# Optimization experiments

Measured on AMD Instinct MI355X. Metric: run time of the kernel, lower is better.

## Reference

```python
import jax, jax.numpy as jnp
import numpy as np

B, T, Q, H = 128, 50, 1024, 256
MAX_STEP = 50
TEMP = 0.5
SUP_W, DIST_W, EMBED_W, LOSS_WEIGHT = 1.0, 0.01, 1.0, 1.0
BLUR, DIAMETER, REACH, SCALING, P = 0.005, 1.0, 500.0, 0.5, 2
NEG = -1e9


def _softmin(eps, C, h):
    # h: log-weights + potential/eps over the second axis of C
    return -eps * jax.nn.logsumexp(h[None, :] - C / eps, axis=1)


def _sqcost(u, v):
    sq = jnp.sum(u * u, -1)[:, None] + jnp.sum(v * v, -1)[None, :] - 2.0 * (u @ v.T)
    return 0.5 * jnp.maximum(sq, 0.0)  # geomloss p=2 cost: |x-y|^2 / 2


def sinkhorn_divergence(x, y):
    # geomloss SamplesLoss('sinkhorn', p=2, blur=0.005, diameter=1, reach=500),
    # tensorized, debiased, unbalanced, eps-scaling schedule.
    N, M = x.shape[0], y.shape[0]
    a_log = jnp.full((N,), -np.log(float(N)), dtype=x.dtype)
    b_log = jnp.full((M,), -np.log(float(M)), dtype=x.dtype)
    Cxy, Cyx = _sqcost(x, y), _sqcost(y, x)
    Cxx, Cyy = _sqcost(x, x), _sqcost(y, y)
    rho = REACH ** P
    eps_final = BLUR ** P
    eps_list = []
    e = DIAMETER ** P
    while e > eps_final:
        eps_list.append(e)
        e = e * (SCALING ** P)
    eps_list.append(eps_final)
    f_ab = jnp.zeros((N,), x.dtype)
    g_ab = jnp.zeros((M,), x.dtype)
    f_aa = jnp.zeros((N,), x.dtype)
    g_bb = jnp.zeros((M,), x.dtype)
    for eps in eps_list:  # static schedule (~9 steps)
        damp = 1.0 / (1.0 + eps / rho)
        ft = damp * _softmin(eps, Cxy, b_log + g_ab / eps)
        gt = damp * _softmin(eps, Cyx, a_log + f_ab / eps)
        faa = 0.5 * (f_aa + damp * _softmin(eps, Cxx, a_log + f_aa / eps))
        gbb = 0.5 * (g_bb + damp * _softmin(eps, Cyy, b_log + g_bb / eps))
        f_ab, g_ab, f_aa, g_bb = ft, gt, faa, gbb
    w = rho + eps_final / 2.0  # UnbalancedWeight
    a_w, b_w = jnp.exp(a_log), jnp.exp(b_log)
    return (jnp.sum(a_w * w * (jnp.exp(-f_aa / rho) - jnp.exp(-f_ab / rho)))
            + jnp.sum(b_w * w * (jnp.exp(-g_bb / rho) - jnp.exp(-g_ab / rho))))


def _forward(lc, lt, le, ltc, ltt, lte, ohs, oht, ods, odt, batch):
    p_c, p_t, p_e = lc / TEMP, lt / TEMP, le / TEMP
    q_c, q_t, q_e = ltc / TEMP, ltt / TEMP, lte / TEMP
    flat = lambda z: z.reshape(z.shape[0], -1)
    loss_kd = (sinkhorn_divergence(flat(p_c), flat(q_c))
               + sinkhorn_divergence(flat(p_t), flat(q_t))
               + sinkhorn_divergence(flat(p_e), flat(q_e)))
    S = MAX_STEP - 1
    delta = batch[:, :, :Q] + batch[:, :, Q:]  # [B,T,Q] question one-hots
    a = jnp.floor(((batch[:, :, :Q] - batch[:, :, Q:]).sum(-1) + 1.0) / 2.0)[:, 1:1 + S]  # [B,S] correctness
    dsh = delta[:, 1:1 + S]  # [B,S,Q]
    # diagonal of p[:S] @ delta[1:].T == per-step gather of next question's logit
    pc = jnp.einsum('bsq,bsq->bs', p_c[:, :S], dsh)
    pt = jnp.einsum('bsq,bsq->bs', p_t[:, :S], dsh)
    pe = jnp.einsum('bsq,bsq->bs', p_e[:, :S], dsh)
    idx = jnp.arange(S)
    last = jnp.max(jnp.where(pc > 0, idx[None, :], -1), axis=1)  # last i with pc[i] > 0
    L = jnp.where(last >= 0, last + 1, S)  # no break => keep full length
    mask = idx[None, :] < L[:, None]
    def ce(logits):
        m = jnp.where(mask, logits, NEG)
        lsm = m - jax.nn.logsumexp(m, axis=1, keepdims=True)
        return -jnp.sum(jnp.where(mask, a * lsm, 0.0))  # soft-target CE, summed over students
    loss_sup = ce(pt) + ce(pc) + ce(pe)
    embed = 0.5 * (jnp.sum((ohs - oht) ** 2) + jnp.sum((ods - odt) ** 2))
    total = LOSS_WEIGHT * (SUP_W * loss_sup + DIST_W * loss_kd + EMBED_W * embed)
    return total.reshape(1)


def setup_inputs():
    key = jax.random.key(0)
    ks = jax.random.split(key, 12)
    rn = lambda k, s: jax.random.normal(k, s, dtype=jnp.float32)
    qid = jax.random.randint(ks[10], (B, T), 0, Q)
    correct = jax.random.randint(ks[11], (B, T), 0, 2).astype(jnp.float32)
    oh = jax.nn.one_hot(qid, Q, dtype=jnp.float32)
    batch = jnp.concatenate([oh * correct[..., None], oh * (1.0 - correct)[..., None]], axis=-1)
    return {
        'logit_c': rn(ks[0], (B, T, Q)),
        'logit_t': rn(ks[1], (B, T, Q)),
        'logit_ensemble': rn(ks[2], (B, T, Q)),
        'logit_teacher_c': rn(ks[3], (B, T, Q)),
        'logit_teacher_t': rn(ks[4], (B, T, Q)),
        'logit_teacher_ensemble': rn(ks[5], (B, T, Q)),
        'out_h_student': rn(ks[6], (B, T, H)),
        'out_h_teacher': rn(ks[7], (B, T, H)),
        'out_d_student': rn(ks[8], (B, T, H)),
        'out_d_teacher': rn(ks[9], (B, T, H)),
        'batch': batch,
    }


def reference(logit_c, logit_t, logit_ensemble, logit_teacher_c, logit_teacher_t, logit_teacher_ensemble, out_h_student, out_h_teacher, out_d_student, out_d_teacher, batch):
    return _forward(logit_c, logit_t, logit_ensemble, logit_teacher_c, logit_teacher_t, logit_teacher_ensemble, out_h_student, out_h_teacher, out_d_student, out_d_teacher, batch)
```

## Files before the change

kernel.cpp:

```cpp
#include <hip/hip_runtime.h>

#define NB 128
#define T_DIM 50
#define Q_DIM 1024
#define H_DIM 256
#define S_DIM 49
#define K_DIM 51200
#define KCHUNKS 80
#define KC 640
#define BK 64
#define NSTAGE 10
#define GRAM_N (NB * NB)
#define LROWU 36
#define CPAD 132

typedef __attribute__((ext_vector_type(4))) float f32x4;
typedef __attribute__((ext_vector_type(8))) _Float16 half8v;
typedef __attribute__((ext_vector_type(4))) unsigned int uint4v;
typedef __attribute__((ext_vector_type(2))) unsigned int uint2v;
using pk2_t = decltype(__builtin_amdgcn_cvt_pkrtz(0.0f, 0.0f));

union PKU { pk2_t p; unsigned int u; };
union U4H8 { uint4v u; half8v h; };

__device__ inline unsigned short f2bf_rn(float x) {
  union { float f; unsigned int u; } v; v.f = x;
  unsigned int r = v.u + 0x7FFFu + ((v.u >> 16) & 1u);
  return (unsigned short)(r >> 16);
}
__device__ inline float bf2f(unsigned short b) {
  union { float f; unsigned int u; } v; v.u = ((unsigned int)b) << 16;
  return v.f;
}

__global__ __launch_bounds__(1024) void gram_fused_kernel(
    const float* __restrict__ s0, const float* __restrict__ s1, const float* __restrict__ s2,
    const float* __restrict__ t0, const float* __restrict__ t1, const float* __restrict__ t2,
    unsigned short* __restrict__ part) {
  __shared__ unsigned int panA[NB * LROWU];
  __shared__ unsigned int panB[NB * LROWU];

  const int chunk = blockIdx.x;
  const int pair = blockIdx.y;
  const float* S  = (pair == 0) ? s0 : ((pair == 1) ? s1 : s2);
  const float* Tm = (pair == 0) ? t0 : ((pair == 1) ? t1 : t2);

  const int tid = threadIdx.x;
  const int wave = tid >> 6, lane = tid & 63;
  const int wrow = wave >> 2, wcol = wave & 3;
  const int l15 = lane & 15, quad = lane >> 4;

  f32x4 aXY[2][2], aXX[2][2], aYY[2][2];
#pragma unroll
  for (int i = 0; i < 2; i++)
#pragma unroll
    for (int j = 0; j < 2; j++) {
      aXY[i][j] = (f32x4){0.f, 0.f, 0.f, 0.f};
      aXX[i][j] = (f32x4){0.f, 0.f, 0.f, 0.f};
      aYY[i][j] = (f32x4){0.f, 0.f, 0.f, 0.f};
    }

  const int r0 = tid >> 4;
  const int kq = tid & 15;
  const size_t ro0 = (size_t)r0 * K_DIM;
  const size_t ro1 = (size_t)(r0 + 64) * K_DIM;

  const int kbase = chunk * KC;
  f32x4 pre0, pre1, pre2, pre3;

#define ISSUE_LOADS(KPOS)                                    \
  {                                                          \
    const float* pS = S + (KPOS) + kq * 4;                   \
    const float* pT = Tm + (KPOS) + kq * 4;                  \
    pre0 = *(const f32x4*)(pS + ro0);                        \
    pre1 = *(const f32x4*)(pS + ro1);                        \
    pre2 = *(const f32x4*)(pT + ro0);                        \
    pre3 = *(const f32x4*)(pT + ro1);                        \
  }

  ISSUE_LOADS(kbase)

  for (int st = 0; st < NSTAGE; st++) {
    if (st) __syncthreads();
    {
      PKU a, b; uint2v w;
      a.p = __builtin_amdgcn_cvt_pkrtz(pre0[0], pre0[1]);
      b.p = __builtin_amdgcn_cvt_pkrtz(pre0[2], pre0[3]);
      w.x = a.u; w.y = b.u;
      *(uint2v*)&panA[r0 * LROWU + kq * 2] = w;
      a.p = __builtin_amdgcn_cvt_pkrtz(pre1[0], pre1[1]);
      b.p = __builtin_amdgcn_cvt_pkrtz(pre1[2], pre1[3]);
      w.x = a.u; w.y = b.u;
      *(uint2v*)&panA[(r0 + 64) * LROWU + kq * 2] = w;
      a.p = __builtin_amdgcn_cvt_pkrtz(pre2[0], pre2[1]);
      b.p = __builtin_amdgcn_cvt_pkrtz(pre2[2], pre2[3]);
      w.x = a.u; w.y = b.u;
      *(uint2v*)&panB[r0 * LROWU + kq * 2] = w;
      a.p = __builtin_amdgcn_cvt_pkrtz(pre3[0], pre3[1]);
      b.p = __builtin_amdgcn_cvt_pkrtz(pre3[2], pre3[3]);
      w.x = a.u; w.y = b.u;
      *(uint2v*)&panB[(r0 + 64) * LROWU + kq * 2] = w;
    }
    __syncthreads();
    if (st + 1 < NSTAGE) ISSUE_LOADS(kbase + (st + 1) * BK)

#pragma unroll
    for (int ks = 0; ks < 2; ks++) {
      const int kc = ks * 16 + quad * 4;
      half8v as_[2], bs_[2], at_[2], bt_[2];
#pragma unroll
      for (int t = 0; t < 2; t++) {
        U4H8 u;
        u.u = *(const uint4v*)&panA[(wrow * 32 + t * 16 + l15) * LROWU + kc]; as_[t] = u.h;
        u.u = *(const uint4v*)&panA[(wcol * 32 + t * 16 + l15) * LROWU + kc]; bs_[t] = u.h;
        u.u = *(const uint4v*)&panB[(wrow * 32 + t * 16 + l15) * LROWU + kc]; at_[t] = u.h;
        u.u = *(const uint4v*)&panB[(wcol * 32 + t * 16 + l15) * LROWU + kc]; bt_[t] = u.h;
      }
#pragma unroll
      for (int ti = 0; ti < 2; ti++)
#pragma unroll
        for (int tj = 0; tj < 2; tj++) {
          aXY[ti][tj] = __builtin_amdgcn_mfma_f32_16x16x32_f16(as_[ti], bt_[tj], aXY[ti][tj], 0, 0, 0);
          aXX[ti][tj] = __builtin_amdgcn_mfma_f32_16x16x32_f16(as_[ti], bs_[tj], aXX[ti][tj], 0, 0, 0);
          aYY[ti][tj] = __builtin_amdgcn_mfma_f32_16x16x32_f16(at_[ti], bt_[tj], aYY[ti][tj], 0, 0, 0);
        }
    }
  }
#undef ISSUE_LOADS

#pragma unroll
  for (int kind = 0; kind < 3; kind++) {
    unsigned short* out = part + ((size_t)(pair * 3 + kind) * KCHUNKS + chunk) * GRAM_N;
#pragma unroll
    for (int ti = 0; ti < 2; ti++)
#pragma unroll
      for (int tj = 0; tj < 2; tj++) {
        const f32x4 v = (kind == 0) ? aXY[ti][tj] : ((kind == 1) ? aXX[ti][tj] : aYY[ti][tj]);
        const int col = wcol * 32 + tj * 16 + l15;
#pragma unroll
        for (int r = 0; r < 4; r++) {
          const int row = wrow * 32 + ti * 16 + quad * 4 + r;
          out[(size_t)row * NB + col] = f2bf_rn(v[r]);
        }
      }
  }
}

__global__ __launch_bounds__(256) void gram_reduce_kernel(
    const unsigned short* __restrict__ part, float* __restrict__ gram) {
  const int idx = blockIdx.x * 256 + threadIdx.x;
  const int g = idx >> 14;
  const int cell = idx & (GRAM_N - 1);
  const unsigned short* p = part + (size_t)g * KCHUNKS * GRAM_N + cell;
  float s = 0.f;
#pragma unroll
  for (int c = 0; c < KCHUNKS; c++) s += bf2f(p[(size_t)c * GRAM_N]);
  gram[idx] = s;
}

__global__ __launch_bounds__(256, 1) void sinkhorn_part_kernel(
    const float* __restrict__ gram, float* __restrict__ kdpart) {
  const int pair = blockIdx.x, kind = blockIdx.y;
  const float* Gxy = gram + (size_t)(3 * pair + 0) * GRAM_N;
  const float* Gxx = gram + (size_t)(3 * pair + 1) * GRAM_N;
  const float* Gyy = gram + (size_t)(3 * pair + 2) * GRAM_N;

  __shared__ float CL[NB * CPAD];
  __shared__ f32x4 h4a[NB / 4];
  __shared__ f32x4 h4b[NB / 4];
  __shared__ float nx[NB], ny[NB];
  __shared__ float red[256];

  const int tid = threadIdx.x;
  if (tid < NB) {
    nx[tid] = Gxx[tid * (NB + 1)];
    ny[tid] = Gyy[tid * (NB + 1)];
    ((float*)h4a)[tid] = 0.f;
    ((float*)h4b)[tid] = 0.f;
  }
  __syncthreads();

  const float* G  = (kind == 0) ? Gxy : ((kind == 1) ? Gxx : Gyy);
  const float* rn = (kind == 2) ? ny : nx;
  const float* cn = (kind == 1) ? nx : ny;
  for (int idx = tid; idx < GRAM_N; idx += 256) {
    const int i = idx >> 7, j = idx & 127;
    CL[i * CPAD + j] = 2.0f * fmaxf(rn[i] + cn[j] - 2.0f * G[idx], 0.0f);
  }
  __syncthreads();

  const float rho = 250000.0f;
  const float AL = -4.852030263919617f;
  const float LOG2E = 1.4426950408889634f;
  const float LN2 = 0.6931471805599453f;
  const int grp = tid >> 7;
  const int i = tid & 127;
  const bool active = (kind == 0) || (grp == 0);
  const bool colread = (kind == 0) && (grp == 1);

  f32x4 crow[32];
  if (active) {
    if (colread) {
#pragma unroll
      for (int jj = 0; jj < 32; jj++) {
        f32x4 v;
        v[0] = CL[(4 * jj + 0) * CPAD + i];
        v[1] = CL[(4 * jj + 1) * CPAD + i];
        v[2] = CL[(4 * jj + 2) * CPAD + i];
        v[3] = CL[(4 * jj + 3) * CPAD + i];
        crow[jj] = v;
      }
    } else {
#pragma unroll
      for (int jj = 0; jj < 32; jj++)
        crow[jj] = *(const f32x4*)&CL[i * CPAD + 4 * jj];
    }
  }

  float eps = 1.0f;
  for (int it = 0; it < 9; it++) {
    if (it == 8) eps = 2.5e-5f;
    const float inv_eps = 1.0f / eps;
    const float damp = 1.0f / (1.0f + eps / rho);
    const float ebl = eps * AL;

    float newp = 0.f;
    if (active) {
      const f32x4* h = (kind == 0 && grp == 0) ? h4b : h4a;
      f32x4 m4 = (f32x4){-3.0e38f, -3.0e38f, -3.0e38f, -3.0e38f};
#pragma unroll
      for (int jj = 0; jj < 32; jj++) {
        const f32x4 u = h[jj] - crow[jj];
        m4[0] = fmaxf(m4[0], u[0]); m4[1] = fmaxf(m4[1], u[1]);
        m4[2] = fmaxf(m4[2], u[2]); m4[3] = fmaxf(m4[3], u[3]);
      }
      const float m = fmaxf(fmaxf(m4[0], m4[1]), fmaxf(m4[2], m4[3]));
      const float k = inv_eps * LOG2E;
      f32x4 s4 = (f32x4){0.f, 0.f, 0.f, 0.f};
#pragma unroll
      for (int jj = 0; jj < 32; jj++) {
        const f32x4 u = h[jj] - crow[jj];
        s4[0] += __builtin_exp2f((u[0] - m) * k);
        s4[1] += __builtin_exp2f((u[1] - m) * k);
        s4[2] += __builtin_exp2f((u[2] - m) * k);
        s4[3] += __builtin_exp2f((u[3] - m) * k);
      }
      const float Ssum = (s4[0] + s4[1]) + (s4[2] + s4[3]);
      const float sm = -(m + ebl + eps * (LN2 * __log2f(Ssum)));
      if (kind == 0) newp = damp * sm;
      else           newp = 0.5f * (((const float*)h4a)[i] + damp * sm);
    }
    __syncthreads();
    if (active) {
      if (grp == 0) ((float*)h4a)[i] = newp;
      else          ((float*)h4b)[i] = newp;
    }
    __syncthreads();
    eps *= 0.25f;
  }

  float v = 0.f;
  if (kind == 0) {
    v = (grp == 0) ? -__expf(-((const float*)h4a)[i] / rho)
                   : -__expf(-((const float*)h4b)[i] / rho);
  } else if (grp == 0) {
    v = __expf(-((const float*)h4a)[i] / rho);
  }
  red[tid] = v;
  __syncthreads();
  for (int st = 128; st > 0; st >>= 1) {
    if (tid < st) red[tid] += red[tid + st];
    __syncthreads();
  }
  if (tid == 0) kdpart[pair * 3 + kind] = red[0];
}

__global__ __launch_bounds__(256) void ps_kernel(
    const float* __restrict__ lc, const float* __restrict__ lt, const float* __restrict__ le,
    const float* __restrict__ batch,
    float* __restrict__ pc, float* __restrict__ pt, float* __restrict__ pe,
    float* __restrict__ aarr) {
  const int bs = blockIdx.x;
  const int b = bs / S_DIM, s = bs % S_DIM;
  const float* brow = batch + ((size_t)b * T_DIM + (s + 1)) * (2 * Q_DIM);
  __shared__ int sq;
  __shared__ float sds;
  if (threadIdx.x == 0) sq = 0;
  __syncthreads();
  for (int q = threadIdx.x; q < Q_DIM; q += 256) {
    float d0 = brow[q], d1 = brow[Q_DIM + q];
    if (d0 + d1 > 0.5f) { sq = q; sds = d0 - d1; }
  }
  __syncthreads();
  if (threadIdx.x == 0) {
    const size_t off = ((size_t)b * T_DIM + s) * Q_DIM + sq;
    pc[bs] = 2.0f * lc[off];
    pt[bs] = 2.0f * lt[off];
    pe[bs] = 2.0f * le[off];
    aarr[bs] = (sds > 0.0f) ? 1.0f : 0.0f;
  }
}

__global__ __launch_bounds__(256) void embed_kernel(
    const f32x4* __restrict__ hs, const f32x4* __restrict__ ht,
    const f32x4* __restrict__ ds, const f32x4* __restrict__ dt,
    float* __restrict__ acc) {
  const int N4 = NB * T_DIM * H_DIM / 4;
  float sum = 0.f;
  for (int idx = blockIdx.x * 256 + threadIdx.x; idx < N4; idx += gridDim.x * 256) {
    f32x4 a = hs[idx] - ht[idx];
    f32x4 b = ds[idx] - dt[idx];
    sum += a[0]*a[0] + a[1]*a[1] + a[2]*a[2] + a[3]*a[3]
         + b[0]*b[0] + b[1]*b[1] + b[2]*b[2] + b[3]*b[3];
  }
  for (int off = 32; off > 0; off >>= 1) sum += __shfl_down(sum, off, 64);
  __shared__ float wsum[4];
  const int lane = threadIdx.x & 63, wv = threadIdx.x >> 6;
  if (lane == 0) wsum[wv] = sum;
  __syncthreads();
  if (threadIdx.x == 0) atomicAdd(acc, wsum[0] + wsum[1] + wsum[2] + wsum[3]);
}

__device__ inline float ce_row(const float* __restrict__ x, const float* __restrict__ a, int L) {
  float m = -3.0e38f;
  for (int s = 0; s < L; s++) m = fmaxf(m, x[s]);
  float sum = 0.f;
  for (int s = 0; s < L; s++) sum += __expf(x[s] - m);
  const float lse = m + __logf(sum);
  float loss = 0.f;
  for (int s = 0; s < L; s++) loss += a[s] * (x[s] - lse);
  return -loss;
}

__global__ __launch_bounds__(128) void ce_final_kernel(
    const float* __restrict__ pc, const float* __restrict__ pt, const float* __restrict__ pe,
    const float* __restrict__ aarr, const float* __restrict__ kdpart,
    const float* __restrict__ emb, float* __restrict__ out) {
  const int b = threadIdx.x;
  const float* xc = pc + b * S_DIM;
  const float* xt = pt + b * S_DIM;
  const float* xe = pe + b * S_DIM;
  const float* av = aarr + b * S_DIM;
  int last = -1;
  for (int s = 0; s < S_DIM; s++)
    if (xc[s] > 0.0f) last = s;
  const int L = (last >= 0) ? (last + 1) : S_DIM;
  float loss = ce_row(xt, av, L) + ce_row(xc, av, L) + ce_row(xe, av, L);
  __shared__ float red[128];
  red[b] = loss;
  __syncthreads();
  for (int st = 64; st > 0; st >>= 1) {
    if (b < st) red[b] += red[b + st];
    __syncthreads();
  }
  if (b == 0) {
    float kd = 0.f;
    for (int k = 0; k < 9; k++) kd += kdpart[k];
    out[0] = red[0] + 0.01f * (250000.0000125f / 128.0f) * kd + 0.5f * emb[0];
  }
}

extern "C" void kernel_launch(void* const* d_in, const int* in_sizes, int n_in,
                              void* d_out, int out_size, void* d_ws, size_t ws_size,
                              hipStream_t stream) {
  const float* lc    = (const float*)d_in[0];
  const float* lt    = (const float*)d_in[1];
  const float* le    = (const float*)d_in[2];
  const float* ltc   = (const float*)d_in[3];
  const float* ltt   = (const float*)d_in[4];
  const float* lte   = (const float*)d_in[5];
  const float* ohs   = (const float*)d_in[6];
  const float* oht   = (const float*)d_in[7];
  const float* ods   = (const float*)d_in[8];
  const float* odt   = (const float*)d_in[9];
  const float* batch = (const float*)d_in[10];

  unsigned short* part = (unsigned short*)d_ws;
  float* gram = (float*)(part + (size_t)9 * KCHUNKS * GRAM_N);
  float* pcb  = gram + 9 * GRAM_N;
  float* ptb  = pcb + NB * S_DIM;
  float* peb  = ptb + NB * S_DIM;
  float* ab   = peb + NB * S_DIM;
  float* kdp  = ab + NB * S_DIM;
  float* emb  = kdp + 9;

  hipMemsetAsync(emb, 0, sizeof(float), stream);

  embed_kernel<<<512, 256, 0, stream>>>(
      (const f32x4*)ohs, (const f32x4*)oht, (const f32x4*)ods, (const f32x4*)odt, emb);

  ps_kernel<<<NB * S_DIM, 256, 0, stream>>>(lc, lt, le, batch, pcb, ptb, peb, ab);

  gram_fused_kernel<<<dim3(KCHUNKS, 3), 1024, 0, stream>>>(lc, lt, le, ltc, ltt, lte, part);

  gram_reduce_kernel<<<(9 * GRAM_N) / 256, 256, 0, stream>>>(part, gram);

  sinkhorn_part_kernel<<<dim3(3, 3), 256, 0, stream>>>(gram, kdp);

  ce_final_kernel<<<1, 128, 0, stream>>>(pcb, ptb, peb, ab, kdp, emb, (float*)d_out);
}
```

Measured before the change: 361.8 us.

## Double-buffer gram LDS panels and split K into twice as many chunks

```diff
diff --git a/kernel.cpp b/kernel.cpp
--- a/kernel.cpp
+++ b/kernel.cpp
@@ -6,10 +6,7 @@
 #define H_DIM 256
 #define S_DIM 49
 #define K_DIM 51200
-#define KCHUNKS 80
-#define KC 640
 #define BK 64
-#define NSTAGE 10
 #define GRAM_N (NB * NB)
 #define LROWU 36
 #define CPAD 132
@@ -33,15 +30,15 @@
   return v.f;
 }
 
-__global__ __launch_bounds__(1024) void gram_fused_kernel(
+__global__ __launch_bounds__(1024, 8) void gram_fused_kernel(
     const float* __restrict__ s0, const float* __restrict__ s1, const float* __restrict__ s2,
     const float* __restrict__ t0, const float* __restrict__ t1, const float* __restrict__ t2,
-    unsigned short* __restrict__ part) {
-  __shared__ unsigned int panA[NB * LROWU];
-  __shared__ unsigned int panB[NB * LROWU];
+    unsigned short* __restrict__ part, int kc, int nstage) {
+  __shared__ unsigned int pan[2][2][NB * LROWU];
 
   const int chunk = blockIdx.x;
   const int pair = blockIdx.y;
+  const int kchunks = gridDim.x;
   const float* S  = (pair == 0) ? s0 : ((pair == 1) ? s1 : s2);
   const float* Tm = (pair == 0) ? t0 : ((pair == 1) ? t1 : t2);
 
@@ -65,7 +62,7 @@
   const size_t ro0 = (size_t)r0 * K_DIM;
   const size_t ro1 = (size_t)(r0 + 64) * K_DIM;
 
-  const int kbase = chunk * KC;
+  const int kbase = chunk * kc;
   f32x4 pre0, pre1, pre2, pre3;
 
 #define ISSUE_LOADS(KPOS)                                    \
@@ -80,8 +77,9 @@
 
   ISSUE_LOADS(kbase)
 
-  for (int st = 0; st < NSTAGE; st++) {
-    if (st) __syncthreads();
+  for (int st = 0; st < nstage; st++) {
+    unsigned int* __restrict__ panA = &pan[st & 1][0][0];
+    unsigned int* __restrict__ panB = &pan[st & 1][1][0];
     {
       PKU a, b; uint2v w;
       a.p = __builtin_amdgcn_cvt_pkrtz(pre0[0], pre0[1]);
@@ -102,19 +100,19 @@
       *(uint2v*)&panB[(r0 + 64) * LROWU + kq * 2] = w;
     }
     __syncthreads();
-    if (st + 1 < NSTAGE) ISSUE_LOADS(kbase + (st + 1) * BK)
+    if (st + 1 < nstage) ISSUE_LOADS(kbase + (st + 1) * BK)
 
 #pragma unroll
     for (int ks = 0; ks < 2; ks++) {
-      const int kc = ks * 16 + quad * 4;
+      const int kcc = ks * 16 + quad * 4;
       half8v as_[2], bs_[2], at_[2], bt_[2];
 #pragma unroll
       for (int t = 0; t < 2; t++) {
         U4H8 u;
-        u.u = *(const uint4v*)&panA[(wrow * 32 + t * 16 + l15) * LROWU + kc]; as_[t] = u.h;
-        u.u = *(const uint4v*)&panA[(wcol * 32 + t * 16 + l15) * LROWU + kc]; bs_[t] = u.h;
-        u.u = *(const uint4v*)&panB[(wrow * 32 + t * 16 + l15) * LROWU + kc]; at_[t] = u.h;
-        u.u = *(const uint4v*)&panB[(wcol * 32 + t * 16 + l15) * LROWU + kc]; bt_[t] = u.h;
+        u.u = *(const uint4v*)&panA[(wrow * 32 + t * 16 + l15) * LROWU + kcc]; as_[t] = u.h;
+        u.u = *(const uint4v*)&panA[(wcol * 32 + t * 16 + l15) * LROWU + kcc]; bs_[t] = u.h;
+        u.u = *(const uint4v*)&panB[(wrow * 32 + t * 16 + l15) * LROWU + kcc]; at_[t] = u.h;
+        u.u = *(const uint4v*)&panB[(wcol * 32 + t * 16 + l15) * LROWU + kcc]; bt_[t] = u.h;
       }
 #pragma unroll
       for (int ti = 0; ti < 2; ti++)
@@ -130,7 +128,7 @@
 
 #pragma unroll
   for (int kind = 0; kind < 3; kind++) {
-    unsigned short* out = part + ((size_t)(pair * 3 + kind) * KCHUNKS + chunk) * GRAM_N;
+    unsigned short* out = part + ((size_t)(pair * 3 + kind) * kchunks + chunk) * GRAM_N;
 #pragma unroll
     for (int ti = 0; ti < 2; ti++)
 #pragma unroll
@@ -147,14 +145,13 @@
 }
 
 __global__ __launch_bounds__(256) void gram_reduce_kernel(
-    const unsigned short* __restrict__ part, float* __restrict__ gram) {
+    const unsigned short* __restrict__ part, float* __restrict__ gram, int kchunks) {
   const int idx = blockIdx.x * 256 + threadIdx.x;
   const int g = idx >> 14;
   const int cell = idx & (GRAM_N - 1);
-  const unsigned short* p = part + (size_t)g * KCHUNKS * GRAM_N + cell;
+  const unsigned short* p = part + (size_t)g * kchunks * GRAM_N + cell;
   float s = 0.f;
-#pragma unroll
-  for (int c = 0; c < KCHUNKS; c++) s += bf2f(p[(size_t)c * GRAM_N]);
+  for (int c = 0; c < kchunks; c++) s += bf2f(p[(size_t)c * GRAM_N]);
   gram[idx] = s;
 }
 
@@ -375,8 +372,15 @@
   const float* odt   = (const float*)d_in[9];
   const float* batch = (const float*)d_in[10];
 
+  int kchunks = 160, kc = 320, nstage = 5;
+  {
+    const size_t tail = ((size_t)9 * GRAM_N + 4 * NB * S_DIM + 9 + 1) * sizeof(float);
+    size_t partBytes = (size_t)9 * kchunks * GRAM_N * sizeof(unsigned short);
+    if (partBytes + tail > ws_size) { kchunks = 80; kc = 640; nstage = 10; }
+  }
+
   unsigned short* part = (unsigned short*)d_ws;
-  float* gram = (float*)(part + (size_t)9 * KCHUNKS * GRAM_N);
+  float* gram = (float*)(part + (size_t)9 * kchunks * GRAM_N);
   float* pcb  = gram + 9 * GRAM_N;
   float* ptb  = pcb + NB * S_DIM;
   float* peb  = ptb + NB * S_DIM;
@@ -391,9 +395,9 @@
 
   ps_kernel<<<NB * S_DIM, 256, 0, stream>>>(lc, lt, le, batch, pcb, ptb, peb, ab);
 
-  gram_fused_kernel<<<dim3(KCHUNKS, 3), 1024, 0, stream>>>(lc, lt, le, ltc, ltt, lte, part);
-
-  gram_reduce_kernel<<<(9 * GRAM_N) / 256, 256, 0, stream>>>(part, gram);
+  gram_fused_kernel<<<dim3(kchunks, 3), 1024, 0, stream>>>(lc, lt, le, ltc, ltt, lte, part, kc, nstage);
+
+  gram_reduce_kernel<<<(9 * GRAM_N) / 256, 256, 0, stream>>>(part, gram, kchunks);
 
   sinkhorn_part_kernel<<<dim3(3, 3), 256, 0, stream>>>(gram, kdp);
 
```

Measured after the change: 506.1 us. +39.9%, slower.

## Split fused gram kernel into per-kind blocks with double-buffered LDS

Applied to the files above, without the earlier changes.

```diff
diff --git a/kernel.cpp b/kernel.cpp
--- a/kernel.cpp
+++ b/kernel.cpp
@@ -8,10 +8,10 @@
 #define K_DIM 51200
 #define KCHUNKS 80
 #define KC 640
-#define BK 64
-#define NSTAGE 10
+#define BK32 32
+#define NST 20
 #define GRAM_N (NB * NB)
-#define LROWU 36
+#define LR 18
 #define CPAD 132
 
 typedef __attribute__((ext_vector_type(4))) float f32x4;
@@ -33,117 +33,94 @@
   return v.f;
 }
 
-__global__ __launch_bounds__(1024) void gram_fused_kernel(
+__global__ __launch_bounds__(1024, 8) void gram_unfused_kernel(
     const float* __restrict__ s0, const float* __restrict__ s1, const float* __restrict__ s2,
     const float* __restrict__ t0, const float* __restrict__ t1, const float* __restrict__ t2,
     unsigned short* __restrict__ part) {
-  __shared__ unsigned int panA[NB * LROWU];
-  __shared__ unsigned int panB[NB * LROWU];
-
-  const int chunk = blockIdx.x;
-  const int pair = blockIdx.y;
-  const float* S  = (pair == 0) ? s0 : ((pair == 1) ? s1 : s2);
-  const float* Tm = (pair == 0) ? t0 : ((pair == 1) ? t1 : t2);
+  __shared__ unsigned int pan[2][2][NB * LR];
+
+  const int pk = blockIdx.x;
+  const int chunk = blockIdx.y;
+  const int pair = pk / 3;
+  const int kind = pk - 3 * pair;
+  const float* Sp = (pair == 0) ? s0 : ((pair == 1) ? s1 : s2);
+  const float* Tp = (pair == 0) ? t0 : ((pair == 1) ? t1 : t2);
+  const float* P0 = (kind == 2) ? Tp : Sp;
+  const float* P1 = Tp;
+  const bool dual = (kind == 0);
 
   const int tid = threadIdx.x;
   const int wave = tid >> 6, lane = tid & 63;
   const int wrow = wave >> 2, wcol = wave & 3;
   const int l15 = lane & 15, quad = lane >> 4;
 
-  f32x4 aXY[2][2], aXX[2][2], aYY[2][2];
+  f32x4 acc[2][2];
 #pragma unroll
   for (int i = 0; i < 2; i++)
 #pragma unroll
-    for (int j = 0; j < 2; j++) {
-      aXY[i][j] = (f32x4){0.f, 0.f, 0.f, 0.f};
-      aXX[i][j] = (f32x4){0.f, 0.f, 0.f, 0.f};
-      aYY[i][j] = (f32x4){0.f, 0.f, 0.f, 0.f};
-    }
-
-  const int r0 = tid >> 4;
-  const int kq = tid & 15;
-  const size_t ro0 = (size_t)r0 * K_DIM;
-  const size_t ro1 = (size_t)(r0 + 64) * K_DIM;
-
+    for (int j = 0; j < 2; j++) acc[i][j] = (f32x4){0.f, 0.f, 0.f, 0.f};
+
+  const int r0 = tid >> 3;
+  const int kq = tid & 7;
+  const size_t ro = (size_t)r0 * K_DIM;
   const int kbase = chunk * KC;
-  f32x4 pre0, pre1, pre2, pre3;
-
-#define ISSUE_LOADS(KPOS)                                    \
-  {                                                          \
-    const float* pS = S + (KPOS) + kq * 4;                   \
-    const float* pT = Tm + (KPOS) + kq * 4;                  \
-    pre0 = *(const f32x4*)(pS + ro0);                        \
-    pre1 = *(const f32x4*)(pS + ro1);                        \
-    pre2 = *(const f32x4*)(pT + ro0);                        \
-    pre3 = *(const f32x4*)(pT + ro1);                        \
-  }
-
-  ISSUE_LOADS(kbase)
-
-  for (int st = 0; st < NSTAGE; st++) {
-    if (st) __syncthreads();
+
+  f32x4 pre0, pre1;
+#define ISSUE(KP)                                                     \
+  {                                                                   \
+    pre0 = *(const f32x4*)(P0 + ro + (KP) + kq * 4);                  \
+    if (dual) pre1 = *(const f32x4*)(P1 + ro + (KP) + kq * 4);        \
+  }
+
+  ISSUE(kbase)
+
+  for (int st = 0; st < NST; st++) {
+    const int buf = st & 1;
     {
       PKU a, b; uint2v w;
       a.p = __builtin_amdgcn_cvt_pkrtz(pre0[0], pre0[1]);
       b.p = __builtin_amdgcn_cvt_pkrtz(pre0[2], pre0[3]);
       w.x = a.u; w.y = b.u;
-      *(uint2v*)&panA[r0 * LROWU + kq * 2] = w;
-      a.p = __builtin_amdgcn_cvt_pkrtz(pre1[0], pre1[1]);
-      b.p = __builtin_amdgcn_cvt_pkrtz(pre1[2], pre1[3]);
-      w.x = a.u; w.y = b.u;
-      *(uint2v*)&panA[(r0 + 64) * LROWU + kq * 2] = w;
-      a.p = __builtin_amdgcn_cvt_pkrtz(pre2[0], pre2[1]);
-      b.p = __builtin_amdgcn_cvt_pkrtz(pre2[2], pre2[3]);
-      w.x = a.u; w.y = b.u;
-      *(uint2v*)&panB[r0 * LROWU + kq * 2] = w;
-      a.p = __builtin_amdgcn_cvt_pkrtz(pre3[0], pre3[1]);
-      b.p = __builtin_amdgcn_cvt_pkrtz(pre3[2], pre3[3]);
-      w.x = a.u; w.y = b.u;
-      *(uint2v*)&panB[(r0 + 64) * LROWU + kq * 2] = w;
-    }
-    __syncthreads();
-    if (st + 1 < NSTAGE) ISSUE_LOADS(kbase + (st + 1) * BK)
-
-#pragma unroll
-    for (int ks = 0; ks < 2; ks++) {
-      const int kc = ks * 16 + quad * 4;
-      half8v as_[2], bs_[2], at_[2], bt_[2];
-#pragma unroll
-      for (int t = 0; t < 2; t++) {
-        U4H8 u;
-        u.u = *(const uint4v*)&panA[(wrow * 32 + t * 16 + l15) * LROWU + kc]; as_[t] = u.h;
-        u.u = *(const uint4v*)&panA[(wcol * 32 + t * 16 + l15) * LROWU + kc]; bs_[t] = u.h;
-        u.u = *(const uint4v*)&panB[(wrow * 32 + t * 16 + l15) * LROWU + kc]; at_[t] = u.h;
-        u.u = *(const uint4v*)&panB[(wcol * 32 + t * 16 + l15) * LROWU + kc]; bt_[t] = u.h;
-      }
-#pragma unroll
-      for (int ti = 0; ti < 2; ti++)
-#pragma unroll
-        for (int tj = 0; tj < 2; tj++) {
-          aXY[ti][tj] = __builtin_amdgcn_mfma_f32_16x16x32_f16(as_[ti], bt_[tj], aXY[ti][tj], 0, 0, 0);
-          aXX[ti][tj] = __builtin_amdgcn_mfma_f32_16x16x32_f16(as_[ti], bs_[tj], aXX[ti][tj], 0, 0, 0);
-          aYY[ti][tj] = __builtin_amdgcn_mfma_f32_16x16x32_f16(at_[ti], bt_[tj], aYY[ti][tj], 0, 0, 0);
-        }
-    }
-  }
-#undef ISSUE_LOADS
-
-#pragma unroll
-  for (int kind = 0; kind < 3; kind++) {
-    unsigned short* out = part + ((size_t)(pair * 3 + kind) * KCHUNKS + chunk) * GRAM_N;
+      *(uint2v*)&pan[buf][0][r0 * LR + kq * 2] = w;
+      if (dual) {
+        a.p = __builtin_amdgcn_cvt_pkrtz(pre1[0], pre1[1]);
+        b.p = __builtin_amdgcn_cvt_pkrtz(pre1[2], pre1[3]);
+        w.x = a.u; w.y = b.u;
+        *(uint2v*)&pan[buf][1][r0 * LR + kq * 2] = w;
+      }
+    }
+    if (st + 1 < NST) ISSUE(kbase + (st + 1) * BK32)
+    __syncthreads();
+
+    const unsigned int* pa = &pan[buf][0][0];
+    const unsigned int* pb = &pan[buf][dual ? 1 : 0][0];
+    half8v af[2], bf[2];
+#pragma unroll
+    for (int t = 0; t < 2; t++) {
+      U4H8 u;
+      u.u = *(const uint4v*)&pa[(wrow * 32 + t * 16 + l15) * LR + quad * 4]; af[t] = u.h;
+      u.u = *(const uint4v*)&pb[(wcol * 32 + t * 16 + l15) * LR + quad * 4]; bf[t] = u.h;
+    }
 #pragma unroll
     for (int ti = 0; ti < 2; ti++)
 #pragma unroll
-      for (int tj = 0; tj < 2; tj++) {
-        const f32x4 v = (kind == 0) ? aXY[ti][tj] : ((kind == 1) ? aXX[ti][tj] : aYY[ti][tj]);
-        const int col = wcol * 32 + tj * 16 + l15;
-#pragma unroll
-        for (int r = 0; r < 4; r++) {
-          const int row = wrow * 32 + ti * 16 + quad * 4 + r;
-          out[(size_t)row * NB + col] = f2bf_rn(v[r]);
-        }
-      }
-  }
+      for (int tj = 0; tj < 2; tj++)
+        acc[ti][tj] = __builtin_amdgcn_mfma_f32_16x16x32_f16(af[ti], bf[tj], acc[ti][tj], 0, 0, 0);
+  }
+#undef ISSUE
+
+  unsigned short* out = part + ((size_t)pk * KCHUNKS + chunk) * GRAM_N;
+#pragma unroll
+  for (int ti = 0; ti < 2; ti++)
+#pragma unroll
+    for (int tj = 0; tj < 2; tj++) {
+      const int col = wcol * 32 + tj * 16 + l15;
+#pragma unroll
+      for (int r = 0; r < 4; r++) {
+        const int row = wrow * 32 + ti * 16 + quad * 4 + r;
+        out[(size_t)row * NB + col] = f2bf_rn(acc[ti][tj][r]);
+      }
+    }
 }
 
 __global__ __launch_bounds__(256) void gram_reduce_kernel(
@@ -391,7 +368,7 @@
 
   ps_kernel<<<NB * S_DIM, 256, 0, stream>>>(lc, lt, le, batch, pcb, ptb, peb, ab);
 
-  gram_fused_kernel<<<dim3(KCHUNKS, 3), 1024, 0, stream>>>(lc, lt, le, ltc, ltt, lte, part);
+  gram_unfused_kernel<<<dim3(9, KCHUNKS), 1024, 0, stream>>>(lc, lt, le, ltc, ltt, lte, part);
 
   gram_reduce_kernel<<<(9 * GRAM_N) / 256, 256, 0, stream>>>(part, gram);
 
```

Result: slower. 412.9 us (+14.1%).

## Double-buffer gram LDS panels, stage CE rows in shared memory, widen embed grid

Applied to the files above, without the earlier changes.

```diff
diff --git a/kernel.cpp b/kernel.cpp
--- a/kernel.cpp
+++ b/kernel.cpp
@@ -37,8 +37,7 @@
     const float* __restrict__ s0, const float* __restrict__ s1, const float* __restrict__ s2,
     const float* __restrict__ t0, const float* __restrict__ t1, const float* __restrict__ t2,
     unsigned short* __restrict__ part) {
-  __shared__ unsigned int panA[NB * LROWU];
-  __shared__ unsigned int panB[NB * LROWU];
+  __shared__ unsigned int pan[2][2][NB * LROWU];
 
   const int chunk = blockIdx.x;
   const int pair = blockIdx.y;
@@ -78,55 +77,70 @@
     pre3 = *(const f32x4*)(pT + ro1);                        \
   }
 
+#define CVT_WRITE(BUF)                                       \
+  {                                                          \
+    unsigned int* panA = &pan[BUF][0][0];                    \
+    unsigned int* panB = &pan[BUF][1][0];                    \
+    PKU a, b; uint2v w;                                      \
+    a.p = __builtin_amdgcn_cvt_pkrtz(pre0[0], pre0[1]);      \
+    b.p = __builtin_amdgcn_cvt_pkrtz(pre0[2], pre0[3]);      \
+    w.x = a.u; w.y = b.u;                                    \
+    *(uint2v*)&panA[r0 * LROWU + kq * 2] = w;                \
+    a.p = __builtin_amdgcn_cvt_pkrtz(pre1[0], pre1[1]);      \
+    b.p = __builtin_amdgcn_cvt_pkrtz(pre1[2], pre1[3]);      \
+    w.x = a.u; w.y = b.u;                                    \
+    *(uint2v*)&panA[(r0 + 64) * LROWU + kq * 2] = w;         \
+    a.p = __builtin_amdgcn_cvt_pkrtz(pre2[0], pre2[1]);      \
+    b.p = __builtin_amdgcn_cvt_pkrtz(pre2[2], pre2[3]);      \
+    w.x = a.u; w.y = b.u;                                    \
+    *(uint2v*)&panB[r0 * LROWU + kq * 2] = w;                \
+    a.p = __builtin_amdgcn_cvt_pkrtz(pre3[0], pre3[1]);      \
+    b.p = __builtin_amdgcn_cvt_pkrtz(pre3[2], pre3[3]);      \
+    w.x = a.u; w.y = b.u;                                    \
+    *(uint2v*)&panB[(r0 + 64) * LROWU + kq * 2] = w;         \
+  }
+
   ISSUE_LOADS(kbase)
+  CVT_WRITE(0)
+  __syncthreads();
 
   for (int st = 0; st < NSTAGE; st++) {
-    if (st) __syncthreads();
+    const int buf = st & 1;
+    if (st + 1 < NSTAGE) ISSUE_LOADS(kbase + (st + 1) * BK)
+
     {
-      PKU a, b; uint2v w;
-      a.p = __builtin_amdgcn_cvt_pkrtz(pre0[0], pre0[1]);
-      b.p = __builtin_amdgcn_cvt_pkrtz(pre0[2], pre0[3]);
-      w.x = a.u; w.y = b.u;
-      *(uint2v*)&panA[r0 * LROWU + kq * 2] = w;
-      a.p = __builtin_amdgcn_cvt_pkrtz(pre1[0], pre1[1]);
-      b.p = __builtin_amdgcn_cvt_pkrtz(pre1[2], pre1[3]);
-      w.x = a.u; w.y = b.u;
-      *(uint2v*)&panA[(r0 + 64) * LROWU + kq * 2] = w;
-      a.p = __builtin_amdgcn_cvt_pkrtz(pre2[0], pre2[1]);
-      b.p = __builtin_amdgcn_cvt_pkrtz(pre2[2], pre2[3]);
-      w.x = a.u; w.y = b.u;
-      *(uint2v*)&panB[r0 * LROWU + kq * 2] = w;
-      a.p = __builtin_amdgcn_cvt_pkrtz(pre3[0], pre3[1]);
-      b.p = __builtin_amdgcn_cvt_pkrtz(pre3[2], pre3[3]);
-      w.x = a.u; w.y = b.u;
-      *(uint2v*)&panB[(r0 + 64) * LROWU + kq * 2] = w;
-    }
-    __syncthreads();
-    if (st + 1 < NSTAGE) ISSUE_LOADS(kbase + (st + 1) * BK)
-
-#pragma unroll
-    for (int ks = 0; ks < 2; ks++) {
-      const int kc = ks * 16 + quad * 4;
-      half8v as_[2], bs_[2], at_[2], bt_[2];
-#pragma unroll
-      for (int t = 0; t < 2; t++) {
-        U4H8 u;
-        u.u = *(const uint4v*)&panA[(wrow * 32 + t * 16 + l15) * LROWU + kc]; as_[t] = u.h;
-        u.u = *(const uint4v*)&panA[(wcol * 32 + t * 16 + l15) * LROWU + kc]; bs_[t] = u.h;
-        u.u = *(const uint4v*)&panB[(wrow * 32 + t * 16 + l15) * LROWU + kc]; at_[t] = u.h;
-        u.u = *(const uint4v*)&panB[(wcol * 32 + t * 16 + l15) * LROWU + kc]; bt_[t] = u.h;
+      const unsigned int* panA = &pan[buf][0][0];
+      const unsigned int* panB = &pan[buf][1][0];
+#pragma unroll
+      for (int ks = 0; ks < 2; ks++) {
+        const int kc = ks * 16 + quad * 4;
+        half8v as_[2], bs_[2], at_[2], bt_[2];
+#pragma unroll
+        for (int t = 0; t < 2; t++) {
+          U4H8 u;
+          u.u = *(const uint4v*)&panA[(wrow * 32 + t * 16 + l15) * LROWU + kc]; as_[t] = u.h;
+          u.u = *(const uint4v*)&panA[(wcol * 32 + t * 16 + l15) * LROWU + kc]; bs_[t] = u.h;
+          u.u = *(const uint4v*)&panB[(wrow * 32 + t * 16 + l15) * LROWU + kc]; at_[t] = u.h;
+          u.u = *(const uint4v*)&panB[(wcol * 32 + t * 16 + l15) * LROWU + kc]; bt_[t] = u.h;
+        }
+#pragma unroll
+        for (int ti = 0; ti < 2; ti++)
+#pragma unroll
+          for (int tj = 0; tj < 2; tj++) {
+            aXY[ti][tj] = __builtin_amdgcn_mfma_f32_16x16x32_f16(as_[ti], bt_[tj], aXY[ti][tj], 0, 0, 0);
+            aXX[ti][tj] = __builtin_amdgcn_mfma_f32_16x16x32_f16(as_[ti], bs_[tj], aXX[ti][tj], 0, 0, 0);
+            aYY[ti][tj] = __builtin_amdgcn_mfma_f32_16x16x32_f16(at_[ti], bt_[tj], aYY[ti][tj], 0, 0, 0);
+          }
       }
-#pragma unroll
-      for (int ti = 0; ti < 2; ti++)
-#pragma unroll
-        for (int tj = 0; tj < 2; tj++) {
-          aXY[ti][tj] = __builtin_amdgcn_mfma_f32_16x16x32_f16(as_[ti], bt_[tj], aXY[ti][tj], 0, 0, 0);
-          aXX[ti][tj] = __builtin_amdgcn_mfma_f32_16x16x32_f16(as_[ti], bs_[tj], aXX[ti][tj], 0, 0, 0);
-          aYY[ti][tj] = __builtin_amdgcn_mfma_f32_16x16x32_f16(at_[ti], bt_[tj], aYY[ti][tj], 0, 0, 0);
-        }
+    }
+
+    if (st + 1 < NSTAGE) {
+      CVT_WRITE((st + 1) & 1)
+      __syncthreads();
     }
   }
 #undef ISSUE_LOADS
+#undef CVT_WRITE
 
 #pragma unroll
   for (int kind = 0; kind < 3; kind++) {
@@ -321,31 +335,40 @@
   if (threadIdx.x == 0) atomicAdd(acc, wsum[0] + wsum[1] + wsum[2] + wsum[3]);
 }
 
-__device__ inline float ce_row(const float* __restrict__ x, const float* __restrict__ a, int L) {
-  float m = -3.0e38f;
-  for (int s = 0; s < L; s++) m = fmaxf(m, x[s]);
-  float sum = 0.f;
-  for (int s = 0; s < L; s++) sum += __expf(x[s] - m);
-  const float lse = m + __logf(sum);
-  float loss = 0.f;
-  for (int s = 0; s < L; s++) loss += a[s] * (x[s] - lse);
-  return -loss;
-}
-
 __global__ __launch_bounds__(128) void ce_final_kernel(
     const float* __restrict__ pc, const float* __restrict__ pt, const float* __restrict__ pe,
     const float* __restrict__ aarr, const float* __restrict__ kdpart,
     const float* __restrict__ emb, float* __restrict__ out) {
-  const int b = threadIdx.x;
-  const float* xc = pc + b * S_DIM;
-  const float* xt = pt + b * S_DIM;
-  const float* xe = pe + b * S_DIM;
-  const float* av = aarr + b * S_DIM;
+  __shared__ float sx[4][NB][S_DIM];
+  const int tid = threadIdx.x;
+  for (int idx = tid; idx < NB * S_DIM; idx += 128) {
+    const int b = idx / S_DIM, s = idx - b * S_DIM;
+    sx[0][b][s] = pt[idx];
+    sx[1][b][s] = pc[idx];
+    sx[2][b][s] = pe[idx];
+    sx[3][b][s] = aarr[idx];
+  }
+  __syncthreads();
+
+  const int b = tid;
   int last = -1;
   for (int s = 0; s < S_DIM; s++)
-    if (xc[s] > 0.0f) last = s;
+    if (sx[1][b][s] > 0.0f) last = s;
   const int L = (last >= 0) ? (last + 1) : S_DIM;
-  float loss = ce_row(xt, av, L) + ce_row(xc, av, L) + ce_row(xe, av, L);
+
+  float loss = 0.f;
+#pragma unroll
+  for (int k = 0; k < 3; k++) {
+    float m = -3.0e38f;
+    for (int s = 0; s < L; s++) m = fmaxf(m, sx[k][b][s]);
+    float sum = 0.f;
+    for (int s = 0; s < L; s++) sum += __expf(sx[k][b][s] - m);
+    const float lse = m + __logf(sum);
+    float l = 0.f;
+    for (int s = 0; s < L; s++) l += sx[3][b][s] * (sx[k][b][s] - lse);
+    loss -= l;
+  }
+
   __shared__ float red[128];
   red[b] = loss;
   __syncthreads();
@@ -386,7 +409,7 @@
 
   hipMemsetAsync(emb, 0, sizeof(float), stream);
 
-  embed_kernel<<<512, 256, 0, stream>>>(
+  embed_kernel<<<1600, 256, 0, stream>>>(
       (const f32x4*)ohs, (const f32x4*)oht, (const f32x4*)ods, (const f32x4*)odt, emb);
 
   ps_kernel<<<NB * S_DIM, 256, 0, stream>>>(lc, lt, le, batch, pcb, ptb, peb, ab);
```

Measured after the change: 344.2 us. -4.9%, faster.
